# Kernel optimization log

Hardware: AMD Instinct MI355X
Metric: run time of the kernel (lower is better)

The kernel has to match this reference:

```python
import jax, jax.numpy as jnp
import numpy as np

ALPHA = 0.15
EPSILON = 0.01
RHO = 1e-4
NUM_ITERS = 20  # fixed-iteration unrolling of the data-dependent while-loop (see notes)
N_NODES = 100_000
N_EDGES = 1_600_000
N_SEEDS = 8


def setup_inputs() -> dict:
    rng = np.random.default_rng(0)
    row = rng.integers(0, N_NODES, N_EDGES).astype(np.int32)
    row[:N_NODES] = np.arange(N_NODES, dtype=np.int32)  # every node has >= 1 out-edge
    col = rng.integers(0, N_NODES, N_EDGES).astype(np.int32)
    val = np.ones(N_EDGES, dtype=np.float32)
    deg = np.bincount(row, minlength=N_NODES).astype(np.float32)
    seeds = rng.integers(0, N_NODES, N_SEEDS).astype(np.int32)
    return {
        "adj_row": jnp.asarray(row),
        "adj_col": jnp.asarray(col),
        "adj_val": jnp.asarray(val),
        "out_degree": jnp.asarray(deg),
        "seeds": jnp.asarray(seeds),
    }


def reference(adj_row, adj_col, adj_val, out_degree, seeds):
    n = out_degree.shape[0]
    deg_inv = 1.0 / jnp.maximum(out_degree, 1e-12)
    thresh = (1.0 + EPSILON) * RHO * ALPHA
    half = 0.5 * (1.0 - ALPHA) * deg_inv  # 0.5*(1-alpha)/deg, precomputed [n]

    def single(seed):
        p0 = jnp.zeros((n,), jnp.float32)
        d0 = jnp.zeros((n,), jnp.float32).at[seed].set(-ALPHA * deg_inv[seed])

        def body(carry, _):
            p, d = carry
            active = jnp.max(jnp.abs(d)) > thresh  # while-loop condition
            S = (p - d) >= RHO * ALPHA              # active frontier S_k
            d_pk = jnp.where(S, -(d + RHO * ALPHA), 0.0)  # is_d_pk (zero off S_k)
            # per-edge push: row r gathers v*d_pk[c] / (v*S[c]*deg[c] + 1e-12)
            num = adj_val * d_pk[adj_col]
            den = adj_val * jnp.where(S[adj_col], out_degree[adj_col], 0.0) + 1e-12
            tmp = jax.ops.segment_sum(num / den, adj_row, num_segments=n)
            d_S = (1.0 - deg_inv) * d - RHO * ALPHA * deg_inv - half * d_pk - half * tmp
            d_nb = d - half * tmp  # neighbor update (tmp==0 for non-neighbors)
            d_new = jnp.where(S, d_S, d_nb)
            p_new = jnp.where(S, p + d_pk, p)
            p2 = jnp.where(active, p_new, p)
            d2 = jnp.where(active, d_new, d)
            return (p2, d2), None

        (p, _), _ = jax.lax.scan(body, (p0, d0), None, length=NUM_ITERS)
        return p

    # dense PPR vectors per seed node [N_SEEDS, n] (the torch module returns their nonzero supports)
    return jax.vmap(single)(seeds)
```

## Files before the change

### kernel.cpp

```cpp
#include <hip/hip_runtime.h>

#define ALPHA   0.15f
#define RA      (1e-4f * 0.15f)
#define THRESH  ((1.0f + 0.01f) * 1e-4f * 0.15f)
#define NITER   20
#define NS      8
#define NMIR    64
#define CHW     16
#define BLK     256
#define W4      (BLK / 64)
#define SPAN    384
#define NBIN    8
#define ECHUNK  2048
#define NWMAX   3136

__global__ void init_kernel(const float* __restrict__ deg, const int* __restrict__ seeds,
                            float2* __restrict__ pd, float* __restrict__ dpw,
                            int* __restrict__ cursor, int* __restrict__ flagM,
                            unsigned* __restrict__ maskA, int* __restrict__ blockSums,
                            int N) {
    int idx = blockIdx.x * blockDim.x + threadIdx.x;
    int NW = (N + 31) >> 5;

    int v = (idx < N) ? (int)deg[idx] : 0;
#pragma unroll
    for (int o = 1; o < 64; o <<= 1) v += __shfl_xor(v, o);
    __shared__ int ws[4];
    if ((threadIdx.x & 63) == 0) ws[threadIdx.x >> 6] = v;
    __syncthreads();
    if (threadIdx.x == 0) blockSums[blockIdx.x] = ws[0] + ws[1] + ws[2] + ws[3];

    if (idx < (NITER + 1) * NMIR) {
        int fv = 0;
        if (idx == 0) {
            for (int s = 0; s < NS; ++s) {
                float m = ALPHA / fmaxf(deg[seeds[s]], 1e-12f);
                if (m > THRESH) fv |= (1 << s);
            }
        }
        flagM[idx] = fv;
    }
    if (idx < NW) {
        unsigned mv = 0;
        for (int s = 0; s < NS; ++s) {
            int sd = seeds[s];
            bool S0 = (ALPHA / fmaxf(deg[sd], 1e-12f)) >= RA;
            if (S0 && (sd >> 5) == idx) mv |= (1u << (sd & 31));
        }
        maskA[idx] = mv;
    }
    if (idx >= N) return;
    cursor[idx] = 0;
    float dv[NS];
#pragma unroll
    for (int s = 0; s < NS; ++s) dv[s] = 0.f;
#pragma unroll
    for (int s = 0; s < NS; ++s) {
        if (seeds[s] == idx) dv[s] = -ALPHA / fmaxf(deg[idx], 1e-12f);
    }
    float den = deg[idx] + 1e-12f;
#pragma unroll
    for (int s = 0; s < NS; ++s) {
        pd[idx * NS + s] = make_float2(0.f, dv[s]);
        bool S = (0.f - dv[s]) >= RA;
        dpw[idx * NS + s] = S ? (-(dv[s] + RA) / den) : 0.f;
    }
}

__global__ void scan_sums_kernel(const int* __restrict__ blockSums, int* __restrict__ blockOffs, int nB) {
    __shared__ int buf[1024];
    int t = threadIdx.x;
    int v = (t < nB) ? blockSums[t] : 0;
    buf[t] = v;
    __syncthreads();
    for (int o = 1; o < 1024; o <<= 1) {
        int u = (t >= o) ? buf[t - o] : 0;
        __syncthreads();
        buf[t] += u;
        __syncthreads();
    }
    if (t < nB) blockOffs[t] = buf[t] - v;
}

__global__ void write_offs_kernel(const float* __restrict__ deg, const int* __restrict__ blockOffs,
                                  int* __restrict__ offs, int N, int E) {
    int t = threadIdx.x;
    int i = blockIdx.x * 256 + t;
    int v = (i < N) ? (int)deg[i] : 0;
    __shared__ int buf[256];
    buf[t] = v;
    __syncthreads();
    for (int o = 1; o < 256; o <<= 1) {
        int u = (t >= o) ? buf[t - o] : 0;
        __syncthreads();
        buf[t] += u;
        __syncthreads();
    }
    int excl = buf[t] - v;
    if (i < N) offs[i] = blockOffs[blockIdx.x] + excl;
    if (i == 0) offs[N] = E;
}

__global__ void scatter_kernel(const int* __restrict__ row, const int* __restrict__ col,
                               const int* __restrict__ offs, int* __restrict__ cursor,
                               int* __restrict__ cols, int E, int N) {
    int bin = blockIdx.x & (NBIN - 1);
    int chunk = blockIdx.x >> 3;
    int binW = (N + NBIN - 1) / NBIN;
    int binLo = bin * binW;
    int binHi = min(N, binLo + binW);
    int e = chunk * ECHUNK + threadIdx.x;
#pragma unroll
    for (int i = 0; i < ECHUNK / 256; ++i, e += 256) {
        if (e < E) {
            int r = row[e];
            if (r >= binLo && r < binHi) {
                int pos = offs[r] + atomicAdd(&cursor[r], 1);
                cols[pos] = col[e];
            }
        }
    }
}

__global__ __launch_bounds__(BLK, 6) void update_kernel(
        const int* __restrict__ offs, const int* __restrict__ cols,
        const float* __restrict__ deg,
        const int* __restrict__ flagIn, int* __restrict__ flagOut,
        const unsigned* __restrict__ maskIn, unsigned* __restrict__ maskOut,
        const float* __restrict__ din, float* __restrict__ dout,
        float2* __restrict__ pd, float* __restrict__ outp, int last, int N) {
    __shared__ unsigned smask[NWMAX];
    __shared__ int sColsAll[W4 * SPAN];
    __shared__ unsigned sRow[W4];
    int tid = threadIdx.x;
    int w = tid >> 6;
    int lane = tid & 63;
    int wid = blockIdx.x * W4 + w;
    int base = wid * CHW;
    int NW = (N + 31) >> 5;
    int* sCols = sColsAll + w * SPAN;

    int r4 = lane >> 2;
    int q  = lane & 3;
    int row = base + r4;
    bool rok = row < N;

    int fm = flagIn[lane];
#pragma unroll
    for (int o = 1; o < 64; o <<= 1) fm |= __shfl_xor(fm, o);

    if (fm == 0) {
        if (last && rok) {
            float4 pv4 = ((const float4*)(pd + (size_t)row * NS))[q];
            outp[(2 * q + 0) * (size_t)N + row] = pv4.x;
            outp[(2 * q + 1) * (size_t)N + row] = pv4.z;
        }
        return;
    }

    for (int i = tid; i < NW; i += BLK) smask[i] = maskIn[i];
    __syncthreads();

    int offv = 0;
    if (lane <= CHW) offv = offs[min(base + lane, N)];
    int off0 = __shfl(offv, 0);
    int span = __shfl(offv, CHW) - off0;
    int e0 = __shfl(offv, r4);
    int e1 = __shfl(offv, r4 + 1);
    int rel = e0 - off0, ndg = e1 - e0;

    bool fits = (span <= SPAN);
    if (fits) {
        for (int i = lane; i < span; i += 64) {
            int cc = cols[off0 + i];
            sCols[i] = ((smask[cc >> 5] >> (cc & 31)) & 1u) ? cc : -1;
        }
    }

    int mx = ndg;
#pragma unroll
    for (int o = 1; o < 64; o <<= 1) mx = max(mx, __shfl_xor(mx, o));

    float dg = 1.0f;
    float4 pdv = make_float4(0.f, 0.f, 0.f, 0.f);
    if (rok) {
        dg = deg[row];
        pdv = ((const float4*)(pd + (size_t)row * NS))[q];
    }

    float a0 = 0.f, a1 = 0.f;
    const float2* din2 = (const float2*)din;
    if (fits) {
#pragma unroll 8
        for (int i = 0; i < mx; ++i) {
            int cc = (i < ndg) ? sCols[rel + i] : -1;
            if (cc >= 0) {
                float2 v = din2[(size_t)cc * 4 + q];
                a0 += v.x; a1 += v.y;
            }
        }
    } else {
        for (int i = 0; i < mx; ++i) {
            if (i < ndg) {
                int cc = cols[e0 + i];
                if ((smask[cc >> 5] >> (cc & 31)) & 1u) {
                    float2 v = din2[(size_t)cc * 4 + q];
                    a0 += v.x; a1 += v.y;
                }
            }
        }
    }

    float di = 1.0f / fmaxf(dg, 1e-12f);
    float hf = 0.5f * (1.0f - ALPHA) * di;
    float den = dg + 1e-12f;

    float p0 = pdv.x, d0 = pdv.y, p1 = pdv.z, d1 = pdv.w;
    float w0, w1;
    unsigned fireN = 0, nzN = 0;
    bool chg = false;

#define UPD(PK, DK, AK, B, WK) { \
        bool S = (PK - DK) >= RA; \
        float dpkv = S ? -(DK + RA) : 0.f; \
        float dS  = (1.0f - di) * DK - RA * di - hf * dpkv - hf * AK; \
        float dnb = DK - hf * AK; \
        bool aa = (fm >> (2 * q + B)) & 1; \
        float nd2 = aa ? (S ? dS : dnb) : DK; \
        float np2 = aa ? (S ? PK + dpkv : PK) : PK; \
        bool S2 = (np2 - nd2) >= RA; \
        WK = S2 ? (-(nd2 + RA) / den) : 0.f; \
        if (aa && (S || AK != 0.f)) chg = true; \
        if (aa && fabsf(nd2) > THRESH) fireN |= 1u << B; \
        if (WK != 0.f) nzN |= 1u << B; \
        PK = np2; DK = nd2; }
    UPD(p0, d0, a0, 0, w0)
    UPD(p1, d1, a1, 1, w1)
#undef UPD

    if (last) {
        if (rok) {
            outp[(2 * q + 0) * (size_t)N + row] = p0;
            outp[(2 * q + 1) * (size_t)N + row] = p1;
        }
    } else {
        int nzl = (nzN != 0) ? 1 : 0;
        nzl |= __shfl_xor(nzl, 1);
        nzl |= __shfl_xor(nzl, 2);
        if (rok && chg) {
            ((float4*)(pd + (size_t)row * NS))[q] = make_float4(p0, d0, p1, d1);
        }
        if (rok && nzl) {
            ((float2*)(dout + (size_t)row * NS))[q] = make_float2(w0, w1);
        }
        int rnv = __shfl(nzl, (lane & 15) * 4);
        unsigned long long bw = __ballot(lane < 16 && rnv);
        if (lane == 0) sRow[w] = (unsigned)(bw & 0xFFFFull);
        __syncthreads();
        if (tid < 2) {
            unsigned wv = sRow[2 * tid] | (sRow[2 * tid + 1] << 16);
            int word = blockIdx.x * 2 + tid;
            if (word < NW) maskOut[word] = wv;
        }

        int wm = 0;
        unsigned long long bb0 = __ballot(fireN & 1);
        unsigned long long bb1 = __ballot((fireN >> 1) & 1);
#pragma unroll
        for (int qq = 0; qq < 4; ++qq) {
            if (bb0 & (0x1111111111111111ull << qq)) wm |= 1 << (2 * qq);
            if (bb1 & (0x1111111111111111ull << qq)) wm |= 1 << (2 * qq + 1);
        }
        if (wm && lane == 0) {
            int hsh = wid & (NMIR - 1);
            int cur = __hip_atomic_load(&flagOut[hsh], __ATOMIC_RELAXED,
                                        __HIP_MEMORY_SCOPE_AGENT);
            if ((cur & wm) != wm) atomicOr(&flagOut[hsh], wm);
        }
    }
}

extern "C" void kernel_launch(void* const* d_in, const int* in_sizes, int n_in,
                              void* d_out, int out_size, void* d_ws, size_t ws_size,
                              hipStream_t stream) {
    const int*   adj_row = (const int*)  d_in[0];
    const int*   adj_col = (const int*)  d_in[1];
    const float* deg     = (const float*)d_in[3];
    const int*   seeds   = (const int*)  d_in[4];
    const int E = in_sizes[0];
    const int N = in_sizes[3];
    float* out = (float*)d_out;

    char* base = (char*)d_ws;
    size_t off = 0;
    auto carve = [&](size_t bytes) -> void* {
        off = (off + 255) & ~(size_t)255;
        void* ptr = base + off;
        off += bytes;
        return ptr;
    };
    float2*   pd     = (float2*)  carve((size_t)N * NS * 8);
    float*    dpwB   = (float*)   carve((size_t)N * NS * 4);
    int*      cols   = (int*)     carve((size_t)(E + SPAN) * 4);
    int*      offs   = (int*)     carve((size_t)(N + 1) * 4);
    int*      cursor = (int*)     carve((size_t)N * 4);
    int*      bsums  = (int*)     carve((size_t)1024 * 4);
    int*      boffs  = (int*)     carve((size_t)1024 * 4);
    int*      flagM  = (int*)     carve((size_t)(NITER + 1) * NMIR * 4);
    unsigned* maskA  = (unsigned*)carve((size_t)NWMAX * 4);
    unsigned* maskB  = (unsigned*)carve((size_t)NWMAX * 4);
    float*    dpwA   = out;

    int nb = (N + 255) / 256;
    init_kernel<<<nb, 256, 0, stream>>>(deg, seeds, pd, dpwA, cursor, flagM, maskA,
                                        bsums, N);
    scan_sums_kernel<<<1, 1024, 0, stream>>>(bsums, boffs, nb);
    write_offs_kernel<<<nb, 256, 0, stream>>>(deg, boffs, offs, N, E);
    int chunks = (E + ECHUNK - 1) / ECHUNK;
    scatter_kernel<<<chunks * NBIN, 256, 0, stream>>>(adj_row, adj_col, offs, cursor,
                                                      cols, E, N);

    float*    din   = dpwA;
    float*    dout_ = dpwB;
    unsigned* mIn   = maskA;
    unsigned* mOut  = maskB;
    int rowsPerBlk = W4 * CHW;
    int ub = (N + rowsPerBlk - 1) / rowsPerBlk;
    for (int k = 0; k < NITER; ++k) {
        int last = (k == NITER - 1) ? 1 : 0;
        update_kernel<<<ub, BLK, 0, stream>>>(offs, cols, deg,
                                              flagM + k * NMIR, flagM + (k + 1) * NMIR,
                                              mIn, mOut, din, dout_, pd, out, last, N);
        float* t = din; din = dout_; dout_ = t;
        unsigned* mt = mIn; mIn = mOut; mOut = mt;
    }
}
```

Before: 370.7 us.

## Replace bitmask frontier with compacted remap and dense delta array

Replaces the per-iteration frontier bitmask, which every block had to load into shared memory, with a per-node remap index into a compacted array of nonzero push values. Nonzero rows are assigned slots through a wave-level ballot plus one global atomicAdd per wave, so the gathers touch a dense, smaller working set. This removes the shared mask fill and a block barrier, and raises launch bounds to 8 waves per SIMD now that shared memory use is lower. In exchange it adds a global atomic per wave, a remap write for every row each iteration, and an extra remapIn load for each neighbor column.

```diff
diff --git a/kernel.cpp b/kernel.cpp
--- a/kernel.cpp
+++ b/kernel.cpp
@@ -12,15 +12,13 @@
 #define SPAN    384
 #define NBIN    8
 #define ECHUNK  2048
-#define NWMAX   3136
 
 __global__ void init_kernel(const float* __restrict__ deg, const int* __restrict__ seeds,
-                            float2* __restrict__ pd, float* __restrict__ dpw,
-                            int* __restrict__ cursor, int* __restrict__ flagM,
-                            unsigned* __restrict__ maskA, int* __restrict__ blockSums,
-                            int N) {
+                            float2* __restrict__ pd, float* __restrict__ dincA,
+                            int* __restrict__ remapA, int* __restrict__ cursor,
+                            int* __restrict__ flagM, int* __restrict__ gcnt,
+                            int* __restrict__ blockSums, int N) {
     int idx = blockIdx.x * blockDim.x + threadIdx.x;
-    int NW = (N + 31) >> 5;
 
     int v = (idx < N) ? (int)deg[idx] : 0;
 #pragma unroll
@@ -30,6 +28,7 @@
     __syncthreads();
     if (threadIdx.x == 0) blockSums[blockIdx.x] = ws[0] + ws[1] + ws[2] + ws[3];
 
+    if (idx < NITER) gcnt[idx] = 0;
     if (idx < (NITER + 1) * NMIR) {
         int fv = 0;
         if (idx == 0) {
@@ -40,31 +39,42 @@
         }
         flagM[idx] = fv;
     }
-    if (idx < NW) {
-        unsigned mv = 0;
+    if (idx >= N) return;
+    cursor[idx] = 0;
+
+    float dv[NS];
+    bool  Sv[NS];
+    bool nz = false;
+#pragma unroll
+    for (int s = 0; s < NS; ++s) dv[s] = 0.f;
+#pragma unroll
+    for (int s = 0; s < NS; ++s) {
+        if (seeds[s] == idx) dv[s] = -ALPHA / fmaxf(deg[idx], 1e-12f);
+    }
+    float den = deg[idx] + 1e-12f;
+#pragma unroll
+    for (int s = 0; s < NS; ++s) {
+        pd[idx * NS + s] = make_float2(0.f, dv[s]);
+        Sv[s] = (0.f - dv[s]) >= RA;
+        if (Sv[s]) nz = true;
+    }
+    int rmp = -1;
+    if (nz) {
+        int rank = 0;
         for (int s = 0; s < NS; ++s) {
             int sd = seeds[s];
-            bool S0 = (ALPHA / fmaxf(deg[sd], 1e-12f)) >= RA;
-            if (S0 && (sd >> 5) == idx) mv |= (1u << (sd & 31));
-        }
-        maskA[idx] = mv;
-    }
-    if (idx >= N) return;
-    cursor[idx] = 0;
-    float dv[NS];
-#pragma unroll
-    for (int s = 0; s < NS; ++s) dv[s] = 0.f;
-#pragma unroll
-    for (int s = 0; s < NS; ++s) {
-        if (seeds[s] == idx) dv[s] = -ALPHA / fmaxf(deg[idx], 1e-12f);
-    }
-    float den = deg[idx] + 1e-12f;
-#pragma unroll
-    for (int s = 0; s < NS; ++s) {
-        pd[idx * NS + s] = make_float2(0.f, dv[s]);
-        bool S = (0.f - dv[s]) >= RA;
-        dpw[idx * NS + s] = S ? (-(dv[s] + RA) / den) : 0.f;
-    }
+            bool first = true;
+            for (int t = 0; t < s; ++t) if (seeds[t] == sd) first = false;
+            if (first && sd < idx) {
+                if ((ALPHA / fmaxf(deg[sd], 1e-12f)) >= RA) rank++;
+            }
+        }
+        rmp = rank;
+#pragma unroll
+        for (int s = 0; s < NS; ++s)
+            dincA[(size_t)rank * NS + s] = Sv[s] ? (-(dv[s] + RA) / den) : 0.f;
+    }
+    remapA[idx] = rmp;
 }
 
 __global__ void scan_sums_kernel(const int* __restrict__ blockSums, int* __restrict__ blockOffs, int nB) {
@@ -122,22 +132,20 @@
     }
 }
 
-__global__ __launch_bounds__(BLK, 6) void update_kernel(
+__global__ __launch_bounds__(BLK, 8) void update_kernel(
         const int* __restrict__ offs, const int* __restrict__ cols,
         const float* __restrict__ deg,
         const int* __restrict__ flagIn, int* __restrict__ flagOut,
-        const unsigned* __restrict__ maskIn, unsigned* __restrict__ maskOut,
-        const float* __restrict__ din, float* __restrict__ dout,
+        const int* __restrict__ remapIn, int* __restrict__ remapOut,
+        const float* __restrict__ dincIn, float* __restrict__ dincOut,
+        int* __restrict__ gc,
         float2* __restrict__ pd, float* __restrict__ outp, int last, int N) {
-    __shared__ unsigned smask[NWMAX];
     __shared__ int sColsAll[W4 * SPAN];
-    __shared__ unsigned sRow[W4];
     int tid = threadIdx.x;
     int w = tid >> 6;
     int lane = tid & 63;
     int wid = blockIdx.x * W4 + w;
     int base = wid * CHW;
-    int NW = (N + 31) >> 5;
     int* sCols = sColsAll + w * SPAN;
 
     int r4 = lane >> 2;
@@ -157,9 +165,6 @@
         }
         return;
     }
-
-    for (int i = tid; i < NW; i += BLK) smask[i] = maskIn[i];
-    __syncthreads();
 
     int offv = 0;
     if (lane <= CHW) offv = offs[min(base + lane, N)];
@@ -173,7 +178,7 @@
     if (fits) {
         for (int i = lane; i < span; i += 64) {
             int cc = cols[off0 + i];
-            sCols[i] = ((smask[cc >> 5] >> (cc & 31)) & 1u) ? cc : -1;
+            sCols[i] = remapIn[cc];
         }
     }
 
@@ -189,7 +194,7 @@
     }
 
     float a0 = 0.f, a1 = 0.f;
-    const float2* din2 = (const float2*)din;
+    const float2* din2 = (const float2*)dincIn;
     if (fits) {
 #pragma unroll 8
         for (int i = 0; i < mx; ++i) {
@@ -202,8 +207,8 @@
     } else {
         for (int i = 0; i < mx; ++i) {
             if (i < ndg) {
-                int cc = cols[e0 + i];
-                if ((smask[cc >> 5] >> (cc & 31)) & 1u) {
+                int cc = remapIn[cols[e0 + i]];
+                if (cc >= 0) {
                     float2 v = din2[(size_t)cc * 4 + q];
                     a0 += v.x; a1 += v.y;
                 }
@@ -247,20 +252,19 @@
         int nzl = (nzN != 0) ? 1 : 0;
         nzl |= __shfl_xor(nzl, 1);
         nzl |= __shfl_xor(nzl, 2);
-        if (rok && chg) {
-            ((float4*)(pd + (size_t)row * NS))[q] = make_float4(p0, d0, p1, d1);
-        }
-        if (rok && nzl) {
-            ((float2*)(dout + (size_t)row * NS))[q] = make_float2(w0, w1);
-        }
-        int rnv = __shfl(nzl, (lane & 15) * 4);
-        unsigned long long bw = __ballot(lane < 16 && rnv);
-        if (lane == 0) sRow[w] = (unsigned)(bw & 0xFFFFull);
-        __syncthreads();
-        if (tid < 2) {
-            unsigned wv = sRow[2 * tid] | (sRow[2 * tid + 1] << 16);
-            int word = blockIdx.x * 2 + tid;
-            if (word < NW) maskOut[word] = wv;
+
+        unsigned long long bal = __ballot(q == 0 && rok && nzl);
+        int cnt = __popcll(bal);
+        int bidx = 0;
+        if (lane == 0 && cnt) bidx = atomicAdd(gc, cnt);
+        bidx = __shfl(bidx, 0);
+        int rank = __popcll(bal & ((1ull << (4 * r4)) - 1));
+
+        if (rok) {
+            int cidx = bidx + rank;
+            if (q == 0) remapOut[row] = nzl ? cidx : -1;
+            if (nzl) ((float2*)dincOut)[(size_t)cidx * 4 + q] = make_float2(w0, w1);
+            if (chg) ((float4*)(pd + (size_t)row * NS))[q] = make_float4(p0, d0, p1, d1);
         }
 
         int wm = 0;
@@ -299,39 +303,41 @@
         off += bytes;
         return ptr;
     };
-    float2*   pd     = (float2*)  carve((size_t)N * NS * 8);
-    float*    dpwB   = (float*)   carve((size_t)N * NS * 4);
-    int*      cols   = (int*)     carve((size_t)(E + SPAN) * 4);
-    int*      offs   = (int*)     carve((size_t)(N + 1) * 4);
-    int*      cursor = (int*)     carve((size_t)N * 4);
-    int*      bsums  = (int*)     carve((size_t)1024 * 4);
-    int*      boffs  = (int*)     carve((size_t)1024 * 4);
-    int*      flagM  = (int*)     carve((size_t)(NITER + 1) * NMIR * 4);
-    unsigned* maskA  = (unsigned*)carve((size_t)NWMAX * 4);
-    unsigned* maskB  = (unsigned*)carve((size_t)NWMAX * 4);
-    float*    dpwA   = out;
+    float2* pd     = (float2*)carve((size_t)N * NS * 8);
+    float*  dincB  = (float*) carve((size_t)N * NS * 4);
+    int*    cols   = (int*)   carve((size_t)(E + SPAN) * 4);
+    int*    offs   = (int*)   carve((size_t)(N + 1) * 4);
+    int*    cursor = (int*)   carve((size_t)N * 4);
+    int*    bsums  = (int*)   carve((size_t)1024 * 4);
+    int*    boffs  = (int*)   carve((size_t)1024 * 4);
+    int*    flagM  = (int*)   carve((size_t)(NITER + 1) * NMIR * 4);
+    int*    remapA = (int*)   carve((size_t)N * 4);
+    int*    remapB = (int*)   carve((size_t)N * 4);
+    int*    gcnt   = (int*)   carve((size_t)NITER * 4);
+    float*  dincA  = out;
 
     int nb = (N + 255) / 256;
-    init_kernel<<<nb, 256, 0, stream>>>(deg, seeds, pd, dpwA, cursor, flagM, maskA,
-                                        bsums, N);
+    init_kernel<<<nb, 256, 0, stream>>>(deg, seeds, pd, dincA, remapA, cursor,
+                                        flagM, gcnt, bsums, N);
     scan_sums_kernel<<<1, 1024, 0, stream>>>(bsums, boffs, nb);
     write_offs_kernel<<<nb, 256, 0, stream>>>(deg, boffs, offs, N, E);
     int chunks = (E + ECHUNK - 1) / ECHUNK;
     scatter_kernel<<<chunks * NBIN, 256, 0, stream>>>(adj_row, adj_col, offs, cursor,
                                                       cols, E, N);
 
-    float*    din   = dpwA;
-    float*    dout_ = dpwB;
-    unsigned* mIn   = maskA;
-    unsigned* mOut  = maskB;
+    float* din   = dincA;
+    float* dout_ = dincB;
+    int*   rIn   = remapA;
+    int*   rOut  = remapB;
     int rowsPerBlk = W4 * CHW;
     int ub = (N + rowsPerBlk - 1) / rowsPerBlk;
     for (int k = 0; k < NITER; ++k) {
         int last = (k == NITER - 1) ? 1 : 0;
         update_kernel<<<ub, BLK, 0, stream>>>(offs, cols, deg,
                                               flagM + k * NMIR, flagM + (k + 1) * NMIR,
-                                              mIn, mOut, din, dout_, pd, out, last, N);
+                                              rIn, rOut, din, dout_, gcnt + k,
+                                              pd, out, last, N);
         float* t = din; din = dout_; dout_ = t;
-        unsigned* mt = mIn; mIn = mOut; mOut = mt;
-    }
-}
+        int* rt = rIn; rIn = rOut; rOut = rt;
+    }
+}
```

Measured after the change: 433.6 us. 1.17x slower.
